# Optimization experiments

Hardware: AMD Instinct MI355X
Metric: run time of the kernel (lower is better)

The kernel has to match this reference:

```python
import jax, jax.numpy as jnp
import numpy as np

D_MODEL = 1024
N_HEADS = 16
D_HEAD = D_MODEL // N_HEADS
B, T = 2, 2048


def setup_inputs() -> dict:
    key = jax.random.key(0)
    k1, k2, k3 = jax.random.split(key, 3)
    x = jax.random.normal(k1, (B, T, D_MODEL), dtype=jnp.float32)
    # torch nn.Linear weights: y = x @ W.T, W has shape [out, in]
    W_qkv = jax.random.normal(k2, (3 * D_MODEL, D_MODEL), dtype=jnp.float32) * (1.0 / np.sqrt(D_MODEL))
    W_out = jax.random.normal(k3, (D_MODEL, D_MODEL), dtype=jnp.float32) * (1.0 / np.sqrt(D_MODEL))
    return {"x": x, "W_qkv": W_qkv, "W_out": W_out}


def reference(x, W_qkv, W_out):
    Bb, Tt, Dd = x.shape
    qkv = (x @ W_qkv.T).reshape(Bb, Tt, 3, N_HEADS, D_HEAD)
    q, k, v = qkv[:, :, 0], qkv[:, :, 1], qkv[:, :, 2]  # [B,T,H,d]
    q = q.transpose(0, 2, 1, 3)  # [B,H,T,d]
    k = k.transpose(0, 2, 1, 3)
    v = v.transpose(0, 2, 1, 3)
    scale = 1.0 / np.sqrt(D_HEAD)
    scores = jnp.einsum('bhqd,bhkd->bhqk', q, k) * scale  # [B,H,T,T]
    causal = jnp.tril(jnp.ones((Tt, Tt), dtype=bool))
    scores = jnp.where(causal, scores, -jnp.inf)
    A = jax.nn.softmax(scores, axis=-1)
    AV = jnp.einsum('bhqk,bhkd->bhqd', A, v)
    AAV = jnp.einsum('bhqk,bhkd->bhqd', A, AV)  # twicing correction
    out = 2.0 * AV - AAV  # [B,H,T,d]
    out = out.transpose(0, 2, 1, 3).reshape(Bb, Tt, Dd)
    return out @ W_out.T
```

## Files before the change

kernel.cpp:

```cpp
#include <hip/hip_runtime.h>
#include <hip/hip_bf16.h>

#define T_SEQ  2048
#define DMODEL 1024
#define NH     16
#define DH     64
#define NTOK   4096
#define QSCALE 0.18033688011112042f
#define M_FIX  16.0f

typedef unsigned short u16;
typedef short s16x8 __attribute__((ext_vector_type(8)));
typedef unsigned short u16x8 __attribute__((ext_vector_type(8)));
typedef float f32x4 __attribute__((ext_vector_type(4)));

__device__ __forceinline__ u16 f2bf(float f) {
  unsigned u = __float_as_uint(f);
  u += 0x7FFFu + ((u >> 16) & 1u);
  return (u16)(u >> 16);
}
__device__ __forceinline__ unsigned pk2(float a, float b) {
  __hip_bfloat162 h = __float22bfloat162_rn(make_float2(a, b));
  unsigned u;
  __builtin_memcpy(&u, &h, 4);
  return u;
}
__device__ __forceinline__ unsigned pk2z(float a, float b) {
  return __builtin_amdgcn_perm(__float_as_uint(b), __float_as_uint(a), 0x07060302);
}
__device__ __forceinline__ float bf2f(u16 x) {
  return __uint_as_float(((unsigned)x) << 16);
}
__device__ __forceinline__ void async_cp16(const u16* g, u16* l) {
  __builtin_amdgcn_global_load_lds(
      (const __attribute__((address_space(1))) unsigned*)g,
      (__attribute__((address_space(3))) unsigned*)l, 16, 0, 0);
}

__global__ void cast_to_bf16(const float* __restrict__ in, u16* __restrict__ out, int n4) {
  int i = blockIdx.x * blockDim.x + threadIdx.x;
  if (i >= n4) return;
  float4 v = reinterpret_cast<const float4*>(in)[i];
  ushort4 r;
  r.x = f2bf(v.x); r.y = f2bf(v.y); r.z = f2bf(v.z); r.w = f2bf(v.w);
  reinterpret_cast<ushort4*>(out)[i] = r;
}

__global__ __launch_bounds__(256) void gemm_qkv(
    const u16* __restrict__ A, const u16* __restrict__ Bm,
    u16* __restrict__ outQ, u16* __restrict__ outK, u16* __restrict__ outV) {
  __shared__ __align__(16) u16 SM[16384];
  const int tid = threadIdx.x, wave = tid >> 6, lane = tid & 63;
  const int f15 = lane & 15, quad = lane >> 4;
  const int bm = blockIdx.x * 128, bn = blockIdx.y * 128;
  const int wr = wave >> 1, wc = wave & 1;
  const int K = DMODEL;

  f32x4 acc[4][4] = {};

  const u16* Ag0 = A  + (size_t)(bm + (2 * wave) * 16 + f15) * K + quad * 8;
  const u16* Ag1 = A  + (size_t)(bm + (2 * wave + 1) * 16 + f15) * K + quad * 8;
  const u16* Bg0 = Bm + (size_t)(bn + (2 * wave) * 16 + f15) * K + quad * 8;
  const u16* Bg1 = Bm + (size_t)(bn + (2 * wave + 1) * 16 + f15) * K + quad * 8;
  u16* LA0 = SM + (2 * wave) * 512 + lane * 8;
  u16* LA1 = SM + (2 * wave + 1) * 512 + lane * 8;
  u16* LB0 = SM + 4096 + (2 * wave) * 512 + lane * 8;
  u16* LB1 = SM + 4096 + (2 * wave + 1) * 512 + lane * 8;

  const int KT = K >> 5;
  async_cp16(Ag0, LA0); async_cp16(Ag1, LA1);
  async_cp16(Bg0, LB0); async_cp16(Bg1, LB1);
  __syncthreads();

  for (int kt = 0; kt < KT; kt++) {
    const int buf = kt & 1;
    if (kt + 1 < KT) {
      const int k0 = (kt + 1) * 32;
      const int o = (buf ^ 1) * 8192;
      async_cp16(Ag0 + k0, LA0 + o); async_cp16(Ag1 + k0, LA1 + o);
      async_cp16(Bg0 + k0, LB0 + o); async_cp16(Bg1 + k0, LB1 + o);
    }
    const u16* Af = SM + buf * 8192;
    const u16* Bf = SM + buf * 8192 + 4096;
    s16x8 af[4], bfr[4];
#pragma unroll
    for (int mi = 0; mi < 4; mi++)
      af[mi] = *reinterpret_cast<const s16x8*>(Af + (wr * 4 + mi) * 512 + lane * 8);
#pragma unroll
    for (int ni = 0; ni < 4; ni++)
      bfr[ni] = *reinterpret_cast<const s16x8*>(Bf + (wc * 4 + ni) * 512 + lane * 8);
#pragma unroll
    for (int mi = 0; mi < 4; mi++)
#pragma unroll
      for (int ni = 0; ni < 4; ni++)
        acc[mi][ni] = __builtin_amdgcn_mfma_f32_16x16x32_bf16(af[mi], bfr[ni], acc[mi][ni], 0, 0, 0);
    __syncthreads();
  }

  u16* Cs = SM;
  if (bn < 2048) {
    const float scale = (bn < 1024) ? QSCALE : 1.0f;
#pragma unroll
    for (int h2 = 0; h2 < 2; h2++) {
      __syncthreads();
      if (wr == h2) {
#pragma unroll
        for (int mi = 0; mi < 4; mi++)
#pragma unroll
          for (int ni = 0; ni < 4; ni++) {
            int c = wc * 64 + ni * 16 + f15;
#pragma unroll
            for (int r = 0; r < 4; r++)
              Cs[(mi * 16 + quad * 4 + r) * 136 + c] = f2bf(acc[mi][ni][r] * scale);
          }
      }
      __syncthreads();
      const int row = tid >> 2, cs = (tid & 3) * 32;
      const int gm = bm + h2 * 64 + row;
#pragma unroll
      for (int c8 = 0; c8 < 4; c8++) {
        int gc = bn + cs + c8 * 8;
        u16x8 v = *reinterpret_cast<const u16x8*>(&Cs[row * 136 + cs + c8 * 8]);
        int which = gc >> 10, hh = (gc >> 6) & 15, d = gc & 63;
        u16* dst = (which ? outK : outQ) + ((size_t)hh * NTOK + gm) * 64 + d;
        *reinterpret_cast<u16x8*>(dst) = v;
      }
    }
  } else {
    const int bnV = bn - 2048;
#pragma unroll
    for (int h2 = 0; h2 < 2; h2++) {
      __syncthreads();
      if (wr == h2) {
#pragma unroll
        for (int mi = 0; mi < 4; mi++)
#pragma unroll
          for (int ni = 0; ni < 4; ni++) {
            int c = wc * 64 + ni * 16 + f15;
#pragma unroll
            for (int r = 0; r < 4; r++)
              Cs[(mi * 16 + quad * 4 + r) * 138 + c] = f2bf(acc[mi][ni][r]);
          }
      }
      __syncthreads();
      const int fd = tid >> 3, s8 = (tid & 7) * 8;
      const int tb = ((s8 >> 5) & 1) * 32 + ((s8 >> 3) & 3) * 4;
      const int gmb = bm + h2 * 64;
#pragma unroll
      for (int p = 0; p < 4; p++) {
        const int d = p * 32 + fd;
        u16x8 vv;
#pragma unroll
        for (int j = 0; j < 4; j++) vv[j] = Cs[(tb + j) * 138 + d];
#pragma unroll
        for (int j = 0; j < 4; j++) vv[4 + j] = Cs[(tb + 16 + j) * 138 + d];
        *reinterpret_cast<u16x8*>(outV + (size_t)(bnV + d) * NTOK + gmb + s8) = vv;
      }
    }
  }
}

__global__ __launch_bounds__(256) void gemm_out(
    const u16* __restrict__ A, const u16* __restrict__ Bm, float* __restrict__ outF) {
  __shared__ __align__(16) u16 SM[12288];
  const int tid = threadIdx.x, wave = tid >> 6, lane = tid & 63;
  const int f15 = lane & 15, quad = lane >> 4;
  const int bm = blockIdx.x * 64, bn = blockIdx.y * 128;
  const int wr = wave >> 1, wc = wave & 1;
  const int K = DMODEL, N = DMODEL;

  f32x4 acc[2][4] = {};

  const u16* Ag = A  + (size_t)(bm + wave * 16 + f15) * K + quad * 8;
  const u16* Bg0 = Bm + (size_t)(bn + (2 * wave) * 16 + f15) * K + quad * 8;
  const u16* Bg1 = Bm + (size_t)(bn + (2 * wave + 1) * 16 + f15) * K + quad * 8;
  u16* LA  = SM + wave * 512 + lane * 8;
  u16* LB0 = SM + 2048 + (2 * wave) * 512 + lane * 8;
  u16* LB1 = SM + 2048 + (2 * wave + 1) * 512 + lane * 8;

  const int KT = K >> 5;
  async_cp16(Ag, LA); async_cp16(Bg0, LB0); async_cp16(Bg1, LB1);
  __syncthreads();

  for (int kt = 0; kt < KT; kt++) {
    const int buf = kt & 1;
    if (kt + 1 < KT) {
      const int k0 = (kt + 1) * 32;
      const int o = (buf ^ 1) * 6144;
      async_cp16(Ag + k0, LA + o); async_cp16(Bg0 + k0, LB0 + o); async_cp16(Bg1 + k0, LB1 + o);
    }
    const u16* Af = SM + buf * 6144;
    const u16* Bf = SM + buf * 6144 + 2048;
    s16x8 af[2], bfr[4];
#pragma unroll
    for (int mi = 0; mi < 2; mi++)
      af[mi] = *reinterpret_cast<const s16x8*>(Af + (wr * 2 + mi) * 512 + lane * 8);
#pragma unroll
    for (int ni = 0; ni < 4; ni++)
      bfr[ni] = *reinterpret_cast<const s16x8*>(Bf + (wc * 4 + ni) * 512 + lane * 8);
#pragma unroll
    for (int mi = 0; mi < 2; mi++)
#pragma unroll
      for (int ni = 0; ni < 4; ni++)
        acc[mi][ni] = __builtin_amdgcn_mfma_f32_16x16x32_bf16(af[mi], bfr[ni], acc[mi][ni], 0, 0, 0);
    __syncthreads();
  }

#pragma unroll
  for (int mi = 0; mi < 2; mi++)
#pragma unroll
    for (int ni = 0; ni < 4; ni++)
#pragma unroll
      for (int r = 0; r < 4; r++)
        outF[(size_t)(bm + wr * 32 + mi * 16 + quad * 4 + r) * N + bn + wc * 64 + ni * 16 + f15] =
            acc[mi][ni][r];
}

template <int PASS>
__global__ __launch_bounds__(256) void attn_pass(
    const u16* __restrict__ Qb, const u16* __restrict__ Kb, const u16* __restrict__ Vsrc,
    float* __restrict__ LinvG, u16* __restrict__ Vp2, u16* __restrict__ TW) {
  __shared__ __align__(16) u16 SM[16384];
  const int tid = threadIdx.x, wave = tid >> 6, lane = tid & 63;
  const int f15 = lane & 15, quad = lane >> 4;
  const int bid = blockIdx.x;
  const int y = (bid & 7) * 4 + ((bid >> 3) & 3);
  const int b = y >> 4, h = y & 15;
  const int g = bid >> 5, a = g & 7;
  const int gq = g >> 3;
  const int qt = (gq == 0) ? (31 - a) : (gq == 1) ? (8 + a) : (gq == 2) ? (23 - a) : a;
  const int q0 = qt * 64;
  const int ntiles = qt + 1;
  const size_t qk_base = ((size_t)h * NTOK + (size_t)b * T_SEQ) * 64;
  const size_t vt_base = (size_t)h * 64 * NTOK + (size_t)b * T_SEQ;

  const int qw = q0 + 16 * wave;
  s16x8 qf0, qf1;
  {
    const u16* qp = Qb + qk_base + (size_t)(qw + f15) * 64 + quad * 8;
    qf0 = *reinterpret_cast<const s16x8*>(qp);
    qf1 = *reinterpret_cast<const s16x8*>(qp + 32);
  }
  float invl_r = 0.f;
  if (PASS == 1) invl_r = LinvG[(size_t)y * T_SEQ + qw + f15];

  f32x4 accO[4] = {};
  float l_acc = 0.f;

  const u16* Kg = Kb  + qk_base + (size_t)(wave * 16 + f15) * 64 + quad * 8;
  const u16* Vg = Vsrc + vt_base + (size_t)(wave * 16 + f15) * NTOK + quad * 8;
  u16* LK = SM + (wave * 2) * 512 + lane * 8;
  u16* LV = SM + 4096 + (wave * 2) * 512 + lane * 8;

  async_cp16(Kg, LK); async_cp16(Kg + 32, LK + 512);
  async_cp16(Vg, LV); async_cp16(Vg + 32, LV + 512);
  __syncthreads();

  for (int ti = 0; ti < ntiles; ti++) {
    const int buf = ti & 1;
    if (ti + 1 < ntiles) {
      const int j1 = (ti + 1) * 64;
      const int o = (buf ^ 1) * 8192;
      async_cp16(Kg + (size_t)j1 * 64, LK + o);
      async_cp16(Kg + (size_t)j1 * 64 + 32, LK + o + 512);
      async_cp16(Vg + j1, LV + o);
      async_cp16(Vg + j1 + 32, LV + o + 512);
    }
    const u16* Kf = SM + buf * 8192;
    const u16* Vf = SM + buf * 8192 + 4096;

    f32x4 accS[4] = {};
#pragma unroll
    for (int st = 0; st < 4; st++) {
      s16x8 k0 = *reinterpret_cast<const s16x8*>(Kf + (st * 2) * 512 + lane * 8);
      s16x8 k1 = *reinterpret_cast<const s16x8*>(Kf + (st * 2 + 1) * 512 + lane * 8);
      accS[st] = __builtin_amdgcn_mfma_f32_16x16x32_bf16(k0, qf0, accS[st], 0, 0, 0);
      accS[st] = __builtin_amdgcn_mfma_f32_16x16x32_bf16(k1, qf1, accS[st], 0, 0, 0);
    }
    union pbu { s16x8 v; unsigned u[4]; } pb0, pb1;
    if (ti < qt) {
#pragma unroll
      for (int st = 0; st < 4; st++) {
        float e0 = __builtin_amdgcn_exp2f(accS[st][0] - M_FIX);
        float e1 = __builtin_amdgcn_exp2f(accS[st][1] - M_FIX);
        float e2 = __builtin_amdgcn_exp2f(accS[st][2] - M_FIX);
        float e3 = __builtin_amdgcn_exp2f(accS[st][3] - M_FIX);
        if (PASS == 0) l_acc += (e0 + e1) + (e2 + e3);
        unsigned w0 = pk2z(e0, e1), w1 = pk2z(e2, e3);
        if (st < 2) { pb0.u[(st & 1) * 2] = w0; pb0.u[(st & 1) * 2 + 1] = w1; }
        else        { pb1.u[(st & 1) * 2] = w0; pb1.u[(st & 1) * 2 + 1] = w1; }
      }
    } else {
      const int qrel = 16 * wave + f15;
#pragma unroll
      for (int st = 0; st < 4; st++) {
        const int jb = st * 16 + quad * 4;
        float e0 = (jb + 0 <= qrel) ? __builtin_amdgcn_exp2f(accS[st][0] - M_FIX) : 0.f;
        float e1 = (jb + 1 <= qrel) ? __builtin_amdgcn_exp2f(accS[st][1] - M_FIX) : 0.f;
        float e2 = (jb + 2 <= qrel) ? __builtin_amdgcn_exp2f(accS[st][2] - M_FIX) : 0.f;
        float e3 = (jb + 3 <= qrel) ? __builtin_amdgcn_exp2f(accS[st][3] - M_FIX) : 0.f;
        if (PASS == 0) l_acc += (e0 + e1) + (e2 + e3);
        unsigned w0 = pk2z(e0, e1), w1 = pk2z(e2, e3);
        if (st < 2) { pb0.u[(st & 1) * 2] = w0; pb0.u[(st & 1) * 2 + 1] = w1; }
        else        { pb1.u[(st & 1) * 2] = w0; pb1.u[(st & 1) * 2 + 1] = w1; }
      }
    }
#pragma unroll
    for (int mt = 0; mt < 4; mt++) {
      s16x8 v0 = *reinterpret_cast<const s16x8*>(Vf + (mt * 2) * 512 + lane * 8);
      s16x8 v1 = *reinterpret_cast<const s16x8*>(Vf + (mt * 2 + 1) * 512 + lane * 8);
      accO[mt] = __builtin_amdgcn_mfma_f32_16x16x32_bf16(v0, pb0.v, accO[mt], 0, 0, 0);
      accO[mt] = __builtin_amdgcn_mfma_f32_16x16x32_bf16(v1, pb1.v, accO[mt], 0, 0, 0);
    }
    __syncthreads();
  }

  if (PASS == 0) {
    float l = l_acc;
    l += __shfl_xor(l, 16);
    l += __shfl_xor(l, 32);
    invl_r = 1.0f / l;
    if (quad == 0) LinvG[(size_t)y * T_SEQ + qw + f15] = invl_r;
  }

  if (PASS == 0) {
    u16* E = SM;
    const int ql = 16 * wave + f15;
    const int slot = (ql >> 5) * 32 + ((ql >> 2) & 3) * 8 + ((ql >> 4) & 1) * 4 + (ql & 3);
#pragma unroll
    for (int mt = 0; mt < 4; mt++)
#pragma unroll
      for (int r = 0; r < 4; r++)
        E[(mt * 16 + quad * 4 + r) * 68 + slot] = f2bf(accO[mt][r] * invl_r);
    __syncthreads();
    const int d = tid >> 2, s = (tid & 3) * 16;
    const u16* vg2 = Vsrc + vt_base + (size_t)d * NTOK + q0 + s;
    u16* og = Vp2 + vt_base + (size_t)d * NTOK + q0 + s;
#pragma unroll
    for (int g2 = 0; g2 < 2; g2++) {
      u16x8 vv = *reinterpret_cast<const u16x8*>(vg2 + g2 * 8);
      u16x8 ee = *reinterpret_cast<const u16x8*>(&E[d * 68 + s + g2 * 8]);
      u16x8 oo;
#pragma unroll
      for (int i = 0; i < 8; i++) oo[i] = f2bf(2.0f * bf2f(vv[i]) - bf2f(ee[i]));
      *reinterpret_cast<u16x8*>(og + g2 * 8) = oo;
    }
  } else {
    u16* E2 = SM;
#pragma unroll
    for (int mt = 0; mt < 4; mt++) {
      uint2 w;
      w.x = pk2(accO[mt][0] * invl_r, accO[mt][1] * invl_r);
      w.y = pk2(accO[mt][2] * invl_r, accO[mt][3] * invl_r);
      *reinterpret_cast<uint2*>(&E2[(16 * wave + f15) * 72 + mt * 16 + quad * 4]) = w;
    }
    __syncthreads();
    const int q = tid >> 2, s = (tid & 3) * 16;
    u16* dst = TW + ((size_t)b * T_SEQ + q0 + q) * DMODEL + h * 64 + s;
    *reinterpret_cast<u16x8*>(dst) = *reinterpret_cast<const u16x8*>(&E2[q * 72 + s]);
    *reinterpret_cast<u16x8*>(dst + 8) = *reinterpret_cast<const u16x8*>(&E2[q * 72 + s + 8]);
  }
}

extern "C" void kernel_launch(void* const* d_in, const int* in_sizes, int n_in,
                              void* d_out, int out_size, void* d_ws, size_t ws_size,
                              hipStream_t stream) {
  const float* x    = (const float*)d_in[0];
  const float* Wqkv = (const float*)d_in[1];
  const float* Wout = (const float*)d_in[2];
  float* out = (float*)d_out;
  char* ws = (char*)d_ws;

  u16*   Xb    = (u16*)(ws + 0);
  u16*   Wqkvb = (u16*)(ws + 8388608);
  u16*   Woutb = (u16*)(ws + 14680064);
  u16*   Qb    = (u16*)(ws + 16777216);
  u16*   Kb    = (u16*)(ws + 25165824);
  u16*   Vtp   = (u16*)(ws + 33554432);
  u16*   TW    = (u16*)(ws + 41943040);
  u16*   Vp2   = (u16*)(ws + 50331648);
  float* LinvG = (float*)(ws + 58720256);

  cast_to_bf16<<<4096, 256, 0, stream>>>(x, Xb, 1048576);
  cast_to_bf16<<<3072, 256, 0, stream>>>(Wqkv, Wqkvb, 786432);
  cast_to_bf16<<<1024, 256, 0, stream>>>(Wout, Woutb, 262144);

  gemm_qkv<<<dim3(32, 24), 256, 0, stream>>>(Xb, Wqkvb, Qb, Kb, Vtp);

  attn_pass<0><<<1024, 256, 0, stream>>>(Qb, Kb, Vtp, LinvG, Vp2, nullptr);
  attn_pass<1><<<1024, 256, 0, stream>>>(Qb, Kb, Vp2, LinvG, nullptr, TW);

  gemm_out<<<dim3(64, 8), 256, 0, stream>>>(TW, Woutb, out);
}
```

Baseline: 243.4 us.

## Triple-buffer LDS in QKV and output GEMMs with one barrier per step

Both projection GEMMs move from double to triple-buffered LDS staging, prefetching two k-tiles ahead. Explicit vmcnt waits replace the full __syncthreads, and only one barrier is kept per iteration. The aim is to hide global-load latency and drop one barrier per k-step. In exchange the kernels use more shared memory, which can lower occupancy, and correctness now depends on the hand-counted outstanding-load numbers.

```diff
diff --git a/kernel.cpp b/kernel.cpp
--- a/kernel.cpp
+++ b/kernel.cpp
@@ -49,7 +49,7 @@
 __global__ __launch_bounds__(256) void gemm_qkv(
     const u16* __restrict__ A, const u16* __restrict__ Bm,
     u16* __restrict__ outQ, u16* __restrict__ outK, u16* __restrict__ outV) {
-  __shared__ __align__(16) u16 SM[16384];
+  __shared__ __align__(16) u16 SM[24576];
   const int tid = threadIdx.x, wave = tid >> 6, lane = tid & 63;
   const int f15 = lane & 15, quad = lane >> 4;
   const int bm = blockIdx.x * 128, bn = blockIdx.y * 128;
@@ -70,18 +70,23 @@
   const int KT = K >> 5;
   async_cp16(Ag0, LA0); async_cp16(Ag1, LA1);
   async_cp16(Bg0, LB0); async_cp16(Bg1, LB1);
-  __syncthreads();
-
+  async_cp16(Ag0 + 32, LA0 + 8192); async_cp16(Ag1 + 32, LA1 + 8192);
+  async_cp16(Bg0 + 32, LB0 + 8192); async_cp16(Bg1 + 32, LB1 + 8192);
+
+  int bufr = 0, bufw = 2;
   for (int kt = 0; kt < KT; kt++) {
-    const int buf = kt & 1;
-    if (kt + 1 < KT) {
-      const int k0 = (kt + 1) * 32;
-      const int o = (buf ^ 1) * 8192;
+    if (kt + 1 < KT) asm volatile("s_waitcnt vmcnt(4)" ::: "memory");
+    else             asm volatile("s_waitcnt vmcnt(0)" ::: "memory");
+    __builtin_amdgcn_s_barrier();
+    __builtin_amdgcn_sched_barrier(0);
+    if (kt + 2 < KT) {
+      const int k0 = (kt + 2) * 32;
+      const int o = bufw * 8192;
       async_cp16(Ag0 + k0, LA0 + o); async_cp16(Ag1 + k0, LA1 + o);
       async_cp16(Bg0 + k0, LB0 + o); async_cp16(Bg1 + k0, LB1 + o);
     }
-    const u16* Af = SM + buf * 8192;
-    const u16* Bf = SM + buf * 8192 + 4096;
+    const u16* Af = SM + bufr * 8192;
+    const u16* Bf = Af + 4096;
     s16x8 af[4], bfr[4];
 #pragma unroll
     for (int mi = 0; mi < 4; mi++)
@@ -94,7 +99,8 @@
 #pragma unroll
       for (int ni = 0; ni < 4; ni++)
         acc[mi][ni] = __builtin_amdgcn_mfma_f32_16x16x32_bf16(af[mi], bfr[ni], acc[mi][ni], 0, 0, 0);
-    __syncthreads();
+    bufr = (bufr == 2) ? 0 : bufr + 1;
+    bufw = (bufw == 2) ? 0 : bufw + 1;
   }
 
   u16* Cs = SM;
@@ -162,7 +168,7 @@
 
 __global__ __launch_bounds__(256) void gemm_out(
     const u16* __restrict__ A, const u16* __restrict__ Bm, float* __restrict__ outF) {
-  __shared__ __align__(16) u16 SM[12288];
+  __shared__ __align__(16) u16 SM[18432];
   const int tid = threadIdx.x, wave = tid >> 6, lane = tid & 63;
   const int f15 = lane & 15, quad = lane >> 4;
   const int bm = blockIdx.x * 64, bn = blockIdx.y * 128;
@@ -180,17 +186,21 @@
 
   const int KT = K >> 5;
   async_cp16(Ag, LA); async_cp16(Bg0, LB0); async_cp16(Bg1, LB1);
-  __syncthreads();
-
+  async_cp16(Ag + 32, LA + 6144); async_cp16(Bg0 + 32, LB0 + 6144); async_cp16(Bg1 + 32, LB1 + 6144);
+
+  int bufr = 0, bufw = 2;
   for (int kt = 0; kt < KT; kt++) {
-    const int buf = kt & 1;
-    if (kt + 1 < KT) {
-      const int k0 = (kt + 1) * 32;
-      const int o = (buf ^ 1) * 6144;
+    if (kt + 1 < KT) asm volatile("s_waitcnt vmcnt(3)" ::: "memory");
+    else             asm volatile("s_waitcnt vmcnt(0)" ::: "memory");
+    __builtin_amdgcn_s_barrier();
+    __builtin_amdgcn_sched_barrier(0);
+    if (kt + 2 < KT) {
+      const int k0 = (kt + 2) * 32;
+      const int o = bufw * 6144;
       async_cp16(Ag + k0, LA + o); async_cp16(Bg0 + k0, LB0 + o); async_cp16(Bg1 + k0, LB1 + o);
     }
-    const u16* Af = SM + buf * 6144;
-    const u16* Bf = SM + buf * 6144 + 2048;
+    const u16* Af = SM + bufr * 6144;
+    const u16* Bf = Af + 2048;
     s16x8 af[2], bfr[4];
 #pragma unroll
     for (int mi = 0; mi < 2; mi++)
@@ -203,7 +213,8 @@
 #pragma unroll
       for (int ni = 0; ni < 4; ni++)
         acc[mi][ni] = __builtin_amdgcn_mfma_f32_16x16x32_bf16(af[mi], bfr[ni], acc[mi][ni], 0, 0, 0);
-    __syncthreads();
+    bufr = (bufr == 2) ? 0 : bufr + 1;
+    bufw = (bufw == 2) ? 0 : bufw + 1;
   }
 
 #pragma unroll
```

Result: faster. 233.2 us (-4.2%).
